# Performance work log

Hardware: AMD Instinct MI355X
Metric: run time of the kernel (lower is better)

## Reference

```python
import jax, jax.numpy as jnp
import numpy as np

N_IN = 200000   # active input voxels
N_OUT = 200000  # stride-1 submanifold conv: out_nnz == in_nnz
K_VOL = 27      # 3x3x3 kernel volume
M = 100000      # gathered pairs per kernel offset
C_IN = 64
C_OUT = 64


def setup_inputs() -> dict:
    key = jax.random.key(0)
    k1, k2, k3, k4, k5 = jax.random.split(key, 5)
    in_feats = jax.random.normal(k1, (N_IN, C_IN), dtype=jnp.float32)
    kernel = jax.random.normal(k2, (K_VOL, C_IN, C_OUT), dtype=jnp.float32) * (1.0 / np.sqrt(C_IN))
    bias = jax.random.normal(k3, (C_OUT,), dtype=jnp.float32)
    imap = jax.random.randint(k4, (K_VOL, M), 0, N_IN, dtype=jnp.int32)
    omap = jax.random.randint(k5, (K_VOL, M), 0, N_OUT, dtype=jnp.int32)
    return {"in_feats": in_feats, "kernel": kernel, "bias": bias,
            "imap": imap, "omap": omap}


def reference(in_feats, kernel, bias, imap, omap):
    # Sparse 3D conv: per-kernel-offset gather -> GEMM -> scatter-add.
    # gathered: [K_VOL, M, C_IN]
    gathered = in_feats[imap]
    # per-offset GEMM: [K_VOL, M, C_OUT]
    contrib = jnp.einsum('kmc,kco->kmo', gathered, kernel)
    # scatter-add into output rows: [N_OUT, C_OUT]
    out = jnp.zeros((N_OUT, C_OUT), dtype=in_feats.dtype)
    out = out.at[omap].add(contrib)
    return out + bias
```

## Files before the change

### kernel.cpp

```cpp
#include <hip/hip_runtime.h>
#include <hip/hip_bf16.h>

#define N_IN 200000
#define N_OUT 200000
#define K_VOL 27
#define M_PAIRS 100000
#define C_IN 64
#define C_OUT 64

#define MTILE 64
#define LDS_PAD 72

typedef __attribute__((ext_vector_type(4))) float floatx4;
typedef __attribute__((ext_vector_type(8))) short shortx8;

static __device__ __forceinline__ ushort f32_to_bf16(float f) {
    union { float f; unsigned int u; } x; x.f = f;
    unsigned int u = x.u;
    u += 0x7FFFu + ((u >> 16) & 1u);
    return (ushort)(u >> 16);
}

__global__ void cvt_feats_kernel(const float* __restrict__ src, ushort* __restrict__ dst, int n4) {
    int i = blockIdx.x * blockDim.x + threadIdx.x;
    if (i >= n4) return;
    float4 v = ((const float4*)src)[i];
    ushort4 o;
    o.x = f32_to_bf16(v.x); o.y = f32_to_bf16(v.y);
    o.z = f32_to_bf16(v.z); o.w = f32_to_bf16(v.w);
    ((ushort4*)dst)[i] = o;
}

__global__ void cvt_wt_kernel(const float* __restrict__ w, ushort* __restrict__ wt) {
    int idx = blockIdx.x * blockDim.x + threadIdx.x;
    if (idx >= K_VOL * C_IN * C_OUT) return;
    int k   = idx >> 12;
    int rem = idx & 4095;
    int c   = rem >> 6;
    int o   = rem & 63;
    wt[(k << 12) + (o << 6) + c] = f32_to_bf16(w[idx]);
}

__global__ void init_bias_kernel(const float* __restrict__ bias, float* __restrict__ out, int n4) {
    int i = blockIdx.x * blockDim.x + threadIdx.x;
    if (i >= n4) return;
    int c = (i * 4) & 63;
    float4 b = *(const float4*)(bias + c);
    ((float4*)out)[i] = b;
}

__launch_bounds__(256, 4)
__global__ void spconv_kernel(const ushort* __restrict__ feats,
                              const ushort* __restrict__ wt,
                              const int* __restrict__ imap,
                              const int* __restrict__ omap,
                              float* __restrict__ out) {
    __shared__ ushort Asm[MTILE * LDS_PAD];
    __shared__ ushort Wsm[C_OUT * LDS_PAD];
    __shared__ int omap_s[MTILE];

    const int k   = blockIdx.y;
    const int m0  = blockIdx.x * MTILE;
    const int tid = threadIdx.x;
    const int kM  = k * M_PAIRS;

    #pragma unroll
    for (int p = 0; p < 2; ++p) {
        int cid = tid + p * 256;
        int row = cid >> 3;
        int ch  = cid & 7;
        *(shortx8*)&Wsm[row * LDS_PAD + ch * 8] =
            *(const shortx8*)&wt[(k << 12) + row * 64 + ch * 8];
    }
    #pragma unroll
    for (int p = 0; p < 2; ++p) {
        int cid = tid + p * 256;
        int row = cid >> 3;
        int ch  = cid & 7;
        int m   = m0 + row;
        shortx8 v = {0, 0, 0, 0, 0, 0, 0, 0};
        if (m < M_PAIRS) {
            int g = imap[kM + m];
            v = *(const shortx8*)&feats[(g << 6) + ch * 8];
        }
        *(shortx8*)&Asm[row * LDS_PAD + ch * 8] = v;
    }
    if (tid < MTILE) {
        int m = m0 + tid;
        omap_s[tid] = (m < M_PAIRS) ? omap[kM + m] : -1;
    }
    __syncthreads();

    const int wave = tid >> 6;
    const int lane = tid & 63;
    const int quad = lane >> 4;
    const int l16  = lane & 15;
    const int rbase = wave * 16;

    const shortx8 a0 = *(const shortx8*)&Asm[(rbase + l16) * LDS_PAD + quad * 8];
    const shortx8 a1 = *(const shortx8*)&Asm[(rbase + l16) * LDS_PAD + 32 + quad * 8];

    #pragma unroll
    for (int ct = 0; ct < 4; ++ct) {
        const shortx8 b0 = *(const shortx8*)&Wsm[(ct * 16 + l16) * LDS_PAD + quad * 8];
        const shortx8 b1 = *(const shortx8*)&Wsm[(ct * 16 + l16) * LDS_PAD + 32 + quad * 8];
        floatx4 acc = {0.f, 0.f, 0.f, 0.f};
        acc = __builtin_amdgcn_mfma_f32_16x16x32_bf16(a0, b0, acc, 0, 0, 0);
        acc = __builtin_amdgcn_mfma_f32_16x16x32_bf16(a1, b1, acc, 0, 0, 0);

        const int col = ct * 16 + l16;
        #pragma unroll
        for (int r = 0; r < 4; ++r) {
            int rl = rbase + quad * 4 + r;
            int orow = omap_s[rl];
            if (orow >= 0) atomicAdd(&out[(orow << 6) + col], acc[r]);
        }
    }
}

extern "C" void kernel_launch(void* const* d_in, const int* in_sizes, int n_in,
                              void* d_out, int out_size, void* d_ws, size_t ws_size,
                              hipStream_t stream) {
    const float* in_feats = (const float*)d_in[0];
    const float* kernelw  = (const float*)d_in[1];
    const float* bias     = (const float*)d_in[2];
    const int*   imap     = (const int*)d_in[3];
    const int*   omap     = (const int*)d_in[4];
    float* out = (float*)d_out;

    ushort* feats_bf = (ushort*)d_ws;
    ushort* wt_bf    = (ushort*)((char*)d_ws + (size_t)N_IN * C_IN * 2);

    int n4 = N_IN * C_IN / 4;
    cvt_feats_kernel<<<(n4 + 255) / 256, 256, 0, stream>>>(in_feats, feats_bf, n4);
    cvt_wt_kernel<<<(K_VOL * C_IN * C_OUT + 255) / 256, 256, 0, stream>>>(kernelw, wt_bf);
    int o4 = N_OUT * C_OUT / 4;
    init_bias_kernel<<<(o4 + 255) / 256, 256, 0, stream>>>(bias, out, o4);

    dim3 grid((M_PAIRS + MTILE - 1) / MTILE, K_VOL);
    spconv_kernel<<<grid, 256, 0, stream>>>(feats_bf, wt_bf, imap, omap, out);
}
```

Before: 659.3 us.

## Replace atomic scatter-add with CSR bucketing and segmented reduction

Builds a CSR layout of pairs grouped by output row using a histogram, a three-pass scan and a fill pass. The GEMM kernel then writes bf16 contributions to per-pair slots, and a reduce kernel sums each output row with bias and no float atomics. This removes 172.8M float atomicAdds, but adds several kernels, a 345MB bf16 contribution buffer written and read back, and bf16 rounding of partial products. It only runs when the workspace is large enough; otherwise it falls back to the atomic path.

```diff
diff --git a/kernel.cpp b/kernel.cpp
--- a/kernel.cpp
+++ b/kernel.cpp
@@ -7,9 +7,28 @@
 #define M_PAIRS 100000
 #define C_IN 64
 #define C_OUT 64
+#define NPAIRS (K_VOL * M_PAIRS)
 
 #define MTILE 64
 #define LDS_PAD 72
+
+#define FEATS_OFF   0UL
+#define FEATS_BYTES (200000UL * 64 * 2)
+#define WT_OFF      (FEATS_OFF + FEATS_BYTES)
+#define WT_BYTES    (27UL * 64 * 64 * 2)
+#define OFFS_OFF    (WT_OFF + WT_BYTES)
+#define OFFS_BYTES  (800064UL)
+#define CNT_OFF     (OFFS_OFF + OFFS_BYTES)
+#define CNT_BYTES   (800000UL)
+#define BSUM_OFF    (CNT_OFF + CNT_BYTES)
+#define BSUM_BYTES  (4096UL)
+#define POS_OFF     (BSUM_OFF + BSUM_BYTES)
+#define POS_BYTES   (10800064UL)
+#define CONTRIB_OFF ((POS_OFF + POS_BYTES + 255UL) & ~255UL)
+#define CONTRIB_BYTES (2700000UL * 64 * 2)
+#define WS_NEEDED   (CONTRIB_OFF + CONTRIB_BYTES)
+
+#define SCAN_NB 782
 
 typedef __attribute__((ext_vector_type(4))) float floatx4;
 typedef __attribute__((ext_vector_type(8))) short shortx8;
@@ -19,6 +38,10 @@
     unsigned int u = x.u;
     u += 0x7FFFu + ((u >> 16) & 1u);
     return (ushort)(u >> 16);
+}
+static __device__ __forceinline__ float bf16_to_f32(ushort u) {
+    union { unsigned int ui; float f; } cv; cv.ui = ((unsigned int)u) << 16;
+    return cv.f;
 }
 
 __global__ void cvt_feats_kernel(const float* __restrict__ src, ushort* __restrict__ dst, int n4) {
@@ -41,6 +64,171 @@
     wt[(k << 12) + (o << 6) + c] = f32_to_bf16(w[idx]);
 }
 
+__global__ void hist_kernel(const int* __restrict__ omap, int* __restrict__ counts) {
+    int p = blockIdx.x * blockDim.x + threadIdx.x;
+    if (p >= NPAIRS) return;
+    atomicAdd(&counts[omap[p]], 1);
+}
+
+__global__ void scan1_kernel(const int* __restrict__ counts, int* __restrict__ bsum) {
+    __shared__ int sd[256];
+    int tid = threadIdx.x;
+    int i = blockIdx.x * 256 + tid;
+    sd[tid] = (i < N_OUT) ? counts[i] : 0;
+    __syncthreads();
+    for (int s = 128; s > 0; s >>= 1) {
+        if (tid < s) sd[tid] += sd[tid + s];
+        __syncthreads();
+    }
+    if (tid == 0) bsum[blockIdx.x] = sd[0];
+}
+
+__global__ void scan2_kernel(int* __restrict__ bsum) {
+    __shared__ int sd[1024];
+    int tid = threadIdx.x;
+    int v = (tid < SCAN_NB) ? bsum[tid] : 0;
+    sd[tid] = v;
+    __syncthreads();
+    for (int off = 1; off < 1024; off <<= 1) {
+        int t = (tid >= off) ? sd[tid - off] : 0;
+        __syncthreads();
+        sd[tid] += t;
+        __syncthreads();
+    }
+    if (tid < SCAN_NB) bsum[tid] = sd[tid] - v;
+}
+
+__global__ void scan3_kernel(int* __restrict__ counts_cursor, const int* __restrict__ bsum,
+                             int* __restrict__ offsets) {
+    __shared__ int sd[256];
+    int tid = threadIdx.x;
+    int i = blockIdx.x * 256 + tid;
+    int v = (i < N_OUT) ? counts_cursor[i] : 0;
+    sd[tid] = v;
+    __syncthreads();
+    for (int off = 1; off < 256; off <<= 1) {
+        int t = (tid >= off) ? sd[tid - off] : 0;
+        __syncthreads();
+        sd[tid] += t;
+        __syncthreads();
+    }
+    int excl = sd[tid] - v + bsum[blockIdx.x];
+    if (i <= N_OUT) offsets[i] = excl;
+    if (i < N_OUT) counts_cursor[i] = excl;
+}
+
+__global__ void fill_kernel(const int* __restrict__ omap, int* __restrict__ cursor,
+                            int* __restrict__ pos_of_pair) {
+    int p = blockIdx.x * blockDim.x + threadIdx.x;
+    if (p >= NPAIRS) return;
+    int o = omap[p];
+    pos_of_pair[p] = atomicAdd(&cursor[o], 1);
+}
+
+__launch_bounds__(256, 4)
+__global__ void gemm_scatter_kernel(const ushort* __restrict__ feats,
+                                    const ushort* __restrict__ wt,
+                                    const int* __restrict__ imap,
+                                    const int* __restrict__ pos_of_pair,
+                                    ushort* __restrict__ contrib) {
+    __shared__ ushort Asm[MTILE * LDS_PAD];
+    __shared__ ushort Wsm[C_OUT * LDS_PAD];
+    __shared__ ushort Csm[MTILE * LDS_PAD];
+    __shared__ int pos_s[MTILE];
+
+    const int k   = blockIdx.y;
+    const int m0  = blockIdx.x * MTILE;
+    const int tid = threadIdx.x;
+    const int kM  = k * M_PAIRS;
+
+    #pragma unroll
+    for (int p = 0; p < 2; ++p) {
+        int cid = tid + p * 256;
+        int row = cid >> 3;
+        int ch  = cid & 7;
+        *(shortx8*)&Wsm[row * LDS_PAD + ch * 8] =
+            *(const shortx8*)&wt[(k << 12) + row * 64 + ch * 8];
+    }
+    #pragma unroll
+    for (int p = 0; p < 2; ++p) {
+        int cid = tid + p * 256;
+        int row = cid >> 3;
+        int ch  = cid & 7;
+        int m   = m0 + row;
+        shortx8 v = {0, 0, 0, 0, 0, 0, 0, 0};
+        if (m < M_PAIRS) {
+            int g = imap[kM + m];
+            v = *(const shortx8*)&feats[(g << 6) + ch * 8];
+        }
+        *(shortx8*)&Asm[row * LDS_PAD + ch * 8] = v;
+    }
+    if (tid < MTILE) {
+        int m = m0 + tid;
+        pos_s[tid] = (m < M_PAIRS) ? pos_of_pair[kM + m] : -1;
+    }
+    __syncthreads();
+
+    const int wave = tid >> 6;
+    const int lane = tid & 63;
+    const int quad = lane >> 4;
+    const int l16  = lane & 15;
+    const int rbase = wave * 16;
+
+    const shortx8 a0 = *(const shortx8*)&Asm[(rbase + l16) * LDS_PAD + quad * 8];
+    const shortx8 a1 = *(const shortx8*)&Asm[(rbase + l16) * LDS_PAD + 32 + quad * 8];
+
+    #pragma unroll
+    for (int ct = 0; ct < 4; ++ct) {
+        const shortx8 b0 = *(const shortx8*)&Wsm[(ct * 16 + l16) * LDS_PAD + quad * 8];
+        const shortx8 b1 = *(const shortx8*)&Wsm[(ct * 16 + l16) * LDS_PAD + 32 + quad * 8];
+        floatx4 acc = {0.f, 0.f, 0.f, 0.f};
+        acc = __builtin_amdgcn_mfma_f32_16x16x32_bf16(a0, b0, acc, 0, 0, 0);
+        acc = __builtin_amdgcn_mfma_f32_16x16x32_bf16(a1, b1, acc, 0, 0, 0);
+        const int col = ct * 16 + l16;
+        #pragma unroll
+        for (int r = 0; r < 4; ++r) {
+            int rl = rbase + quad * 4 + r;
+            Csm[rl * LDS_PAD + col] = f32_to_bf16(acc[r]);
+        }
+    }
+    __syncthreads();
+
+    #pragma unroll
+    for (int p = 0; p < 2; ++p) {
+        int cid = tid + p * 256;
+        int row = cid >> 3;
+        int ch  = cid & 7;
+        int pos = pos_s[row];
+        if (pos >= 0) {
+            *(shortx8*)&contrib[(size_t)pos * 64 + ch * 8] =
+                *(const shortx8*)&Csm[row * LDS_PAD + ch * 8];
+        }
+    }
+}
+
+__launch_bounds__(256, 4)
+__global__ void reduce_kernel(const ushort* __restrict__ contrib,
+                              const int* __restrict__ offsets,
+                              const float* __restrict__ bias,
+                              float* __restrict__ out) {
+    int wave = threadIdx.x >> 6;
+    int lane = threadIdx.x & 63;
+    int row  = blockIdx.x * 4 + wave;
+    if (row >= N_OUT) return;
+    int beg = offsets[row];
+    int end = offsets[row + 1];
+    float acc = bias[lane];
+    int j = beg;
+    for (; j + 2 <= end; j += 2) {
+        ushort u0 = contrib[(size_t)j * 64 + lane];
+        ushort u1 = contrib[(size_t)(j + 1) * 64 + lane];
+        acc += bf16_to_f32(u0);
+        acc += bf16_to_f32(u1);
+    }
+    if (j < end) acc += bf16_to_f32(contrib[(size_t)j * 64 + lane]);
+    out[(size_t)row * 64 + lane] = acc;
+}
+
 __global__ void init_bias_kernel(const float* __restrict__ bias, float* __restrict__ out, int n4) {
     int i = blockIdx.x * blockDim.x + threadIdx.x;
     if (i >= n4) return;
@@ -50,11 +238,11 @@
 }
 
 __launch_bounds__(256, 4)
-__global__ void spconv_kernel(const ushort* __restrict__ feats,
-                              const ushort* __restrict__ wt,
-                              const int* __restrict__ imap,
-                              const int* __restrict__ omap,
-                              float* __restrict__ out) {
+__global__ void spconv_push_kernel(const ushort* __restrict__ feats,
+                                   const ushort* __restrict__ wt,
+                                   const int* __restrict__ imap,
+                                   const int* __restrict__ omap,
+                                   float* __restrict__ out) {
     __shared__ ushort Asm[MTILE * LDS_PAD];
     __shared__ ushort Wsm[C_OUT * LDS_PAD];
     __shared__ int omap_s[MTILE];
@@ -107,7 +295,6 @@
         floatx4 acc = {0.f, 0.f, 0.f, 0.f};
         acc = __builtin_amdgcn_mfma_f32_16x16x32_bf16(a0, b0, acc, 0, 0, 0);
         acc = __builtin_amdgcn_mfma_f32_16x16x32_bf16(a1, b1, acc, 0, 0, 0);
-
         const int col = ct * 16 + l16;
         #pragma unroll
         for (int r = 0; r < 4; ++r) {
@@ -128,15 +315,36 @@
     const int*   omap     = (const int*)d_in[4];
     float* out = (float*)d_out;
 
-    ushort* feats_bf = (ushort*)d_ws;
-    ushort* wt_bf    = (ushort*)((char*)d_ws + (size_t)N_IN * C_IN * 2);
+    char* ws = (char*)d_ws;
+    ushort* feats_bf = (ushort*)(ws + FEATS_OFF);
+    ushort* wt_bf    = (ushort*)(ws + WT_OFF);
 
     int n4 = N_IN * C_IN / 4;
     cvt_feats_kernel<<<(n4 + 255) / 256, 256, 0, stream>>>(in_feats, feats_bf, n4);
     cvt_wt_kernel<<<(K_VOL * C_IN * C_OUT + 255) / 256, 256, 0, stream>>>(kernelw, wt_bf);
-    int o4 = N_OUT * C_OUT / 4;
-    init_bias_kernel<<<(o4 + 255) / 256, 256, 0, stream>>>(bias, out, o4);
-
-    dim3 grid((M_PAIRS + MTILE - 1) / MTILE, K_VOL);
-    spconv_kernel<<<grid, 256, 0, stream>>>(feats_bf, wt_bf, imap, omap, out);
-}
+
+    if (ws_size >= WS_NEEDED) {
+        int* offsets = (int*)(ws + OFFS_OFF);
+        int* counts  = (int*)(ws + CNT_OFF);
+        int* bsum    = (int*)(ws + BSUM_OFF);
+        int* pos     = (int*)(ws + POS_OFF);
+        ushort* contrib = (ushort*)(ws + CONTRIB_OFF);
+
+        hipMemsetAsync(counts, 0, CNT_BYTES, stream);
+        hist_kernel<<<(NPAIRS + 255) / 256, 256, 0, stream>>>(omap, counts);
+        scan1_kernel<<<SCAN_NB, 256, 0, stream>>>(counts, bsum);
+        scan2_kernel<<<1, 1024, 0, stream>>>(bsum);
+        scan3_kernel<<<SCAN_NB, 256, 0, stream>>>(counts, bsum, offsets);
+        fill_kernel<<<(NPAIRS + 255) / 256, 256, 0, stream>>>(omap, counts, pos);
+
+        dim3 grid((M_PAIRS + MTILE - 1) / MTILE, K_VOL);
+        gemm_scatter_kernel<<<grid, 256, 0, stream>>>(feats_bf, wt_bf, imap, pos, contrib);
+
+        reduce_kernel<<<(N_OUT + 3) / 4, 256, 0, stream>>>(contrib, offsets, bias, out);
+    } else {
+        int o4 = N_OUT * C_OUT / 4;
+        init_bias_kernel<<<(o4 + 255) / 256, 256, 0, stream>>>(bias, out, o4);
+        dim3 grid((M_PAIRS + MTILE - 1) / MTILE, K_VOL);
+        spconv_push_kernel<<<grid, 256, 0, stream>>>(feats_bf, wt_bf, imap, omap, out);
+    }
+}
```

Result: no change. 659.8 us (+0.1%).

## Accumulate scatter-add in fp16 with packed half2 atomics, finalize to fp32

Applied to the files above, without the earlier changes.

Switches the operands from bf16 to fp16 and scatters results into an fp16 workspace accumulator using packed two-element half atomics. Lanes exchange values with a shuffle so each atomic covers two adjacent columns, which halves the atomic count and the bytes touched. A finalize kernel then converts to fp32 and adds bias. If the workspace is too small, it falls back to the fp32 atomic path. The risk is precision loss and possible overflow from accumulating up to dozens of contributions in fp16.

```diff
diff --git a/kernel.cpp b/kernel.cpp
--- a/kernel.cpp
+++ b/kernel.cpp
@@ -1,5 +1,5 @@
 #include <hip/hip_runtime.h>
-#include <hip/hip_bf16.h>
+#include <hip/hip_fp16.h>
 
 #define N_IN 200000
 #define N_OUT 200000
@@ -7,18 +7,41 @@
 #define M_PAIRS 100000
 #define C_IN 64
 #define C_OUT 64
+#define NPAIRS (K_VOL * M_PAIRS)
 
 #define MTILE 64
 #define LDS_PAD 72
 
 typedef __attribute__((ext_vector_type(4))) float floatx4;
 typedef __attribute__((ext_vector_type(8))) short shortx8;
-
-static __device__ __forceinline__ ushort f32_to_bf16(float f) {
-    union { float f; unsigned int u; } x; x.f = f;
-    unsigned int u = x.u;
-    u += 0x7FFFu + ((u >> 16) & 1u);
-    return (ushort)(u >> 16);
+typedef __attribute__((ext_vector_type(8))) _Float16 halfx8;
+typedef __attribute__((ext_vector_type(2))) _Float16 half2v;
+
+#define FEATS_OFF   0UL
+#define FEATS_BYTES (200000UL * 64 * 2)
+#define WT_OFF      (FEATS_OFF + FEATS_BYTES)
+#define WT_BYTES    (27UL * 64 * 64 * 2)
+#define ACC_OFF     ((WT_OFF + WT_BYTES + 255UL) & ~255UL)
+#define ACC_BYTES   (200000UL * 64 * 2)
+#define WS_NEEDED   (ACC_OFF + ACC_BYTES)
+#define WS_FALLBACK (WT_OFF + WT_BYTES)
+
+static __device__ __forceinline__ ushort f32_to_f16_bits(float f) {
+    union { _Float16 h; ushort u; } cv;
+    cv.h = (_Float16)f;
+    return cv.u;
+}
+
+static __device__ __forceinline__ void atomic_pk_add_f16(ushort* addr, float lo, float hi) {
+    half2v v;
+    v[0] = (_Float16)lo;
+    v[1] = (_Float16)hi;
+#if defined(__has_builtin) && __has_builtin(__builtin_amdgcn_global_atomic_fadd_v2f16)
+    typedef half2v __attribute__((address_space(1))) *as1p;
+    __builtin_amdgcn_global_atomic_fadd_v2f16((as1p)(unsigned long long)addr, v);
+#else
+    unsafeAtomicAdd((__half2*)addr, *(__half2*)&v);
+#endif
 }
 
 __global__ void cvt_feats_kernel(const float* __restrict__ src, ushort* __restrict__ dst, int n4) {
@@ -26,8 +49,8 @@
     if (i >= n4) return;
     float4 v = ((const float4*)src)[i];
     ushort4 o;
-    o.x = f32_to_bf16(v.x); o.y = f32_to_bf16(v.y);
-    o.z = f32_to_bf16(v.z); o.w = f32_to_bf16(v.w);
+    o.x = f32_to_f16_bits(v.x); o.y = f32_to_f16_bits(v.y);
+    o.z = f32_to_f16_bits(v.z); o.w = f32_to_f16_bits(v.w);
     ((ushort4*)dst)[i] = o;
 }
 
@@ -38,23 +61,15 @@
     int rem = idx & 4095;
     int c   = rem >> 6;
     int o   = rem & 63;
-    wt[(k << 12) + (o << 6) + c] = f32_to_bf16(w[idx]);
-}
-
-__global__ void init_bias_kernel(const float* __restrict__ bias, float* __restrict__ out, int n4) {
-    int i = blockIdx.x * blockDim.x + threadIdx.x;
-    if (i >= n4) return;
-    int c = (i * 4) & 63;
-    float4 b = *(const float4*)(bias + c);
-    ((float4*)out)[i] = b;
+    wt[(k << 12) + (o << 6) + c] = f32_to_f16_bits(w[idx]);
 }
 
 __launch_bounds__(256, 4)
-__global__ void spconv_kernel(const ushort* __restrict__ feats,
-                              const ushort* __restrict__ wt,
-                              const int* __restrict__ imap,
-                              const int* __restrict__ omap,
-                              float* __restrict__ out) {
+__global__ void spconv_f16_kernel(const ushort* __restrict__ feats,
+                                  const ushort* __restrict__ wt,
+                                  const int* __restrict__ imap,
+                                  const int* __restrict__ omap,
+                                  ushort* __restrict__ accum) {
     __shared__ ushort Asm[MTILE * LDS_PAD];
     __shared__ ushort Wsm[C_OUT * LDS_PAD];
     __shared__ int omap_s[MTILE];
@@ -96,18 +111,122 @@
     const int quad = lane >> 4;
     const int l16  = lane & 15;
     const int rbase = wave * 16;
-
-    const shortx8 a0 = *(const shortx8*)&Asm[(rbase + l16) * LDS_PAD + quad * 8];
-    const shortx8 a1 = *(const shortx8*)&Asm[(rbase + l16) * LDS_PAD + 32 + quad * 8];
+    const bool even = (l16 & 1) == 0;
+
+    const halfx8 a0 = *(const halfx8*)&Asm[(rbase + l16) * LDS_PAD + quad * 8];
+    const halfx8 a1 = *(const halfx8*)&Asm[(rbase + l16) * LDS_PAD + 32 + quad * 8];
 
     #pragma unroll
     for (int ct = 0; ct < 4; ++ct) {
-        const shortx8 b0 = *(const shortx8*)&Wsm[(ct * 16 + l16) * LDS_PAD + quad * 8];
-        const shortx8 b1 = *(const shortx8*)&Wsm[(ct * 16 + l16) * LDS_PAD + 32 + quad * 8];
+        const halfx8 b0 = *(const halfx8*)&Wsm[(ct * 16 + l16) * LDS_PAD + quad * 8];
+        const halfx8 b1 = *(const halfx8*)&Wsm[(ct * 16 + l16) * LDS_PAD + 32 + quad * 8];
         floatx4 acc = {0.f, 0.f, 0.f, 0.f};
-        acc = __builtin_amdgcn_mfma_f32_16x16x32_bf16(a0, b0, acc, 0, 0, 0);
-        acc = __builtin_amdgcn_mfma_f32_16x16x32_bf16(a1, b1, acc, 0, 0, 0);
-
+        acc = __builtin_amdgcn_mfma_f32_16x16x32_f16(a0, b0, acc, 0, 0, 0);
+        acc = __builtin_amdgcn_mfma_f32_16x16x32_f16(a1, b1, acc, 0, 0, 0);
+
+        float p0 = __shfl_xor(acc[0], 1, 64);
+        float p1 = __shfl_xor(acc[1], 1, 64);
+        float p2 = __shfl_xor(acc[2], 1, 64);
+        float p3 = __shfl_xor(acc[3], 1, 64);
+
+        const int colb = ct * 16 + (l16 & ~1);
+        float lo0, hi0, lo1, hi1;
+        int r0;
+        if (even) { r0 = 0; lo0 = acc[0]; hi0 = p0; lo1 = acc[1]; hi1 = p1; }
+        else      { r0 = 2; lo0 = p2;     hi0 = acc[2]; lo1 = p3; hi1 = acc[3]; }
+
+        int row0 = rbase + quad * 4 + r0;
+        int o0 = omap_s[row0];
+        int o1 = omap_s[row0 + 1];
+        if (o0 >= 0) atomic_pk_add_f16(&accum[(o0 << 6) + colb], lo0, hi0);
+        if (o1 >= 0) atomic_pk_add_f16(&accum[(o1 << 6) + colb], lo1, hi1);
+    }
+}
+
+__global__ void finalize_kernel(const ushort* __restrict__ accum,
+                                const float* __restrict__ bias,
+                                float* __restrict__ out, int n8) {
+    int i = blockIdx.x * blockDim.x + threadIdx.x;
+    if (i >= n8) return;
+    halfx8 h = *(const halfx8*)&accum[(size_t)i * 8];
+    int c = (i * 8) & 63;
+    float4 b0 = *(const float4*)(bias + c);
+    float4 b1 = *(const float4*)(bias + c + 4);
+    float4 o0, o1;
+    o0.x = (float)h[0] + b0.x; o0.y = (float)h[1] + b0.y;
+    o0.z = (float)h[2] + b0.z; o0.w = (float)h[3] + b0.w;
+    o1.x = (float)h[4] + b1.x; o1.y = (float)h[5] + b1.y;
+    o1.z = (float)h[6] + b1.z; o1.w = (float)h[7] + b1.w;
+    ((float4*)out)[(size_t)i * 2]     = o0;
+    ((float4*)out)[(size_t)i * 2 + 1] = o1;
+}
+
+__global__ void init_bias_kernel(const float* __restrict__ bias, float* __restrict__ out, int n4) {
+    int i = blockIdx.x * blockDim.x + threadIdx.x;
+    if (i >= n4) return;
+    int c = (i * 4) & 63;
+    float4 b = *(const float4*)(bias + c);
+    ((float4*)out)[i] = b;
+}
+
+__launch_bounds__(256, 4)
+__global__ void spconv_push_f32_kernel(const ushort* __restrict__ feats,
+                                       const ushort* __restrict__ wt,
+                                       const int* __restrict__ imap,
+                                       const int* __restrict__ omap,
+                                       float* __restrict__ out) {
+    __shared__ ushort Asm[MTILE * LDS_PAD];
+    __shared__ ushort Wsm[C_OUT * LDS_PAD];
+    __shared__ int omap_s[MTILE];
+
+    const int k   = blockIdx.y;
+    const int m0  = blockIdx.x * MTILE;
+    const int tid = threadIdx.x;
+    const int kM  = k * M_PAIRS;
+
+    #pragma unroll
+    for (int p = 0; p < 2; ++p) {
+        int cid = tid + p * 256;
+        int row = cid >> 3;
+        int ch  = cid & 7;
+        *(shortx8*)&Wsm[row * LDS_PAD + ch * 8] =
+            *(const shortx8*)&wt[(k << 12) + row * 64 + ch * 8];
+    }
+    #pragma unroll
+    for (int p = 0; p < 2; ++p) {
+        int cid = tid + p * 256;
+        int row = cid >> 3;
+        int ch  = cid & 7;
+        int m   = m0 + row;
+        shortx8 v = {0, 0, 0, 0, 0, 0, 0, 0};
+        if (m < M_PAIRS) {
+            int g = imap[kM + m];
+            v = *(const shortx8*)&feats[(g << 6) + ch * 8];
+        }
+        *(shortx8*)&Asm[row * LDS_PAD + ch * 8] = v;
+    }
+    if (tid < MTILE) {
+        int m = m0 + tid;
+        omap_s[tid] = (m < M_PAIRS) ? omap[kM + m] : -1;
+    }
+    __syncthreads();
+
+    const int wave = tid >> 6;
+    const int lane = tid & 63;
+    const int quad = lane >> 4;
+    const int l16  = lane & 15;
+    const int rbase = wave * 16;
+
+    const halfx8 a0 = *(const halfx8*)&Asm[(rbase + l16) * LDS_PAD + quad * 8];
+    const halfx8 a1 = *(const halfx8*)&Asm[(rbase + l16) * LDS_PAD + 32 + quad * 8];
+
+    #pragma unroll
+    for (int ct = 0; ct < 4; ++ct) {
+        const halfx8 b0 = *(const halfx8*)&Wsm[(ct * 16 + l16) * LDS_PAD + quad * 8];
+        const halfx8 b1 = *(const halfx8*)&Wsm[(ct * 16 + l16) * LDS_PAD + 32 + quad * 8];
+        floatx4 acc = {0.f, 0.f, 0.f, 0.f};
+        acc = __builtin_amdgcn_mfma_f32_16x16x32_f16(a0, b0, acc, 0, 0, 0);
+        acc = __builtin_amdgcn_mfma_f32_16x16x32_f16(a1, b1, acc, 0, 0, 0);
         const int col = ct * 16 + l16;
         #pragma unroll
         for (int r = 0; r < 4; ++r) {
@@ -128,15 +247,25 @@
     const int*   omap     = (const int*)d_in[4];
     float* out = (float*)d_out;
 
-    ushort* feats_bf = (ushort*)d_ws;
-    ushort* wt_bf    = (ushort*)((char*)d_ws + (size_t)N_IN * C_IN * 2);
+    char* ws = (char*)d_ws;
+    ushort* feats_h = (ushort*)(ws + FEATS_OFF);
+    ushort* wt_h    = (ushort*)(ws + WT_OFF);
 
     int n4 = N_IN * C_IN / 4;
-    cvt_feats_kernel<<<(n4 + 255) / 256, 256, 0, stream>>>(in_feats, feats_bf, n4);
-    cvt_wt_kernel<<<(K_VOL * C_IN * C_OUT + 255) / 256, 256, 0, stream>>>(kernelw, wt_bf);
-    int o4 = N_OUT * C_OUT / 4;
-    init_bias_kernel<<<(o4 + 255) / 256, 256, 0, stream>>>(bias, out, o4);
+    cvt_feats_kernel<<<(n4 + 255) / 256, 256, 0, stream>>>(in_feats, feats_h, n4);
+    cvt_wt_kernel<<<(K_VOL * C_IN * C_OUT + 255) / 256, 256, 0, stream>>>(kernelw, wt_h);
 
     dim3 grid((M_PAIRS + MTILE - 1) / MTILE, K_VOL);
-    spconv_kernel<<<grid, 256, 0, stream>>>(feats_bf, wt_bf, imap, omap, out);
-}
+
+    if (ws_size >= WS_NEEDED) {
+        ushort* accum = (ushort*)(ws + ACC_OFF);
+        hipMemsetAsync(accum, 0, ACC_BYTES, stream);
+        spconv_f16_kernel<<<grid, 256, 0, stream>>>(feats_h, wt_h, imap, omap, accum);
+        int n8 = N_OUT * C_OUT / 8;
+        finalize_kernel<<<(n8 + 255) / 256, 256, 0, stream>>>(accum, bias, out, n8);
+    } else {
+        int o4 = N_OUT * C_OUT / 4;
+        init_bias_kernel<<<(o4 + 255) / 256, 256, 0, stream>>>(bias, out, o4);
+        spconv_push_f32_kernel<<<grid, 256, 0, stream>>>(feats_h, wt_h, imap, omap, out);
+    }
+}
```

Result: no change. 667.3 us (+1.2%).
